# Kernel optimization log

Hardware: AMD Instinct MI355X
Metric: run time of the kernel (lower is better)

The kernel has to match this reference:

```python
import jax, jax.numpy as jnp
import numpy as np

ADAPTIVE_FACTOR = 10  # max(10, num_agents=8)


def _mlp(x, W1, b1, W2, b2, W3, b3):
    h = jax.nn.relu(x @ W1 + b1)
    h = jax.nn.relu(h @ W2 + b2)
    return h @ W3 + b3


def setup_inputs() -> dict:
    key = jax.random.key(0)
    ks = jax.random.split(key, 8)
    B, T, N, D, A = 32, 512, 8, 256, 64
    obs = jax.random.normal(ks[0], (B, T, N, D), dtype=jnp.float32)
    actions = jax.random.uniform(ks[1], (B, T, N, A), dtype=jnp.float32)
    din = D + A
    W1 = jax.random.normal(ks[2], (din, 128), dtype=jnp.float32) / np.sqrt(din)
    b1 = jnp.zeros((128,), dtype=jnp.float32)
    W2 = jax.random.normal(ks[3], (128, 64), dtype=jnp.float32) / np.sqrt(128.0)
    b2 = jnp.zeros((64,), dtype=jnp.float32)
    W3 = jax.random.normal(ks[4], (64, A), dtype=jnp.float32) / np.sqrt(64.0)
    b3 = jnp.zeros((A,), dtype=jnp.float32)
    return {"obs": obs, "actions": actions, "W1": W1, "b1": b1,
            "W2": W2, "b2": b2, "W3": W3, "b3": b3}


def reference(obs, actions, W1, b1, W2, b2, W3, b3):
    # obs: [B,T,N,D], actions: [B,T,N,A]. All agents processed in one batched MLP
    # pass instead of the per-agent Python loop in the original.
    p_with = _mlp(jnp.concatenate([obs, actions], axis=-1), W1, b1, W2, b2, W3, b3)
    p_wo = _mlp(jnp.concatenate([obs, jnp.zeros_like(actions)], axis=-1),
                W1, b1, W2, b2, W3, b3)

    cf_keys = jax.random.split(jax.random.key(42), ADAPTIVE_FACTOR)

    def body(acc, k):
        cf = jax.random.uniform(k, actions.shape, dtype=actions.dtype)
        return acc + _mlp(jnp.concatenate([obs, cf], axis=-1), W1, b1, W2, b2, W3, b3), None

    p_wo, _ = jax.lax.scan(body, p_wo, cf_keys)
    p_wo = p_wo / (ADAPTIVE_FACTOR + 1)

    # F.kl_div(log_softmax(p_with), softmax(p_wo), reduction='none')
    #   = q * (log q - log p)
    logp = jax.nn.log_softmax(p_with, axis=-1)
    logq = jax.nn.log_softmax(p_wo, axis=-1)
    q = jnp.exp(logq)
    influence = q * (logq - logp)          # [B,T,N,A]
    # torch: stack over agents on dim=-1 -> [B,T,A,N], then mean over dim=2 (A)
    return influence.mean(axis=-1)          # [B,T,N]
```

## Files before the change

kernel.cpp:

```cpp
#include <hip/hip_runtime.h>
#include <cstddef>

#define NCF 10

struct TFKeys { unsigned k[2 * NCF]; };

typedef __attribute__((ext_vector_type(8))) _Float16 f16x8;
typedef __attribute__((ext_vector_type(4))) float f32x4;

__host__ __device__ __forceinline__ void tf2x32(unsigned k0, unsigned k1,
                                                unsigned x0, unsigned x1,
                                                unsigned& o0, unsigned& o1) {
  const unsigned ks2 = k0 ^ k1 ^ 0x1BD11BDAu;
  x0 += k0; x1 += k1;
#define TF_R(r) x0 += x1; x1 = (x1 << (r)) | (x1 >> (32 - (r))); x1 ^= x0;
  TF_R(13) TF_R(15) TF_R(26) TF_R(6)
  x0 += k1;  x1 += ks2 + 1u;
  TF_R(17) TF_R(29) TF_R(16) TF_R(24)
  x0 += ks2; x1 += k0 + 2u;
  TF_R(13) TF_R(15) TF_R(26) TF_R(6)
  x0 += k0;  x1 += k1 + 3u;
  TF_R(17) TF_R(29) TF_R(16) TF_R(24)
  x0 += k1;  x1 += ks2 + 4u;
  TF_R(13) TF_R(15) TF_R(26) TF_R(6)
  x0 += ks2; x1 += k0 + 5u;
#undef TF_R
  o0 = x0; o1 = x1;
}

__device__ __forceinline__ float u01(unsigned bits) {
  return __uint_as_float((bits >> 9) | 0x3f800000u) - 1.0f;
}

__device__ __forceinline__ void split44(const float4 a, const float4 b,
                                        f16x8& hh, f16x8& ll) {
  const float v[8] = {a.x, a.y, a.z, a.w, b.x, b.y, b.z, b.w};
#pragma unroll
  for (int e = 0; e < 8; ++e) {
    const _Float16 h = (_Float16)v[e];
    hh[e] = h;
    ll[e] = (_Float16)(v[e] - (float)h);
  }
}

#define MFMA3(acc, ah, al, bh, bl)                                          \
  acc = __builtin_amdgcn_mfma_f32_16x16x32_f16(ah, bh, acc, 0, 0, 0);       \
  acc = __builtin_amdgcn_mfma_f32_16x16x32_f16(ah, bl, acc, 0, 0, 0);       \
  acc = __builtin_amdgcn_mfma_f32_16x16x32_f16(al, bh, acc, 0, 0, 0);

template <int K, int N>
__device__ __forceinline__ void stage_frags(const float* __restrict__ W,
                                            _Float16* fh, _Float16* fl, int t) {
  constexpr int NTN = N / 16;
  for (int i = t; i < K * N; i += 512) {
    const int e = i & 7, lane = (i >> 3) & 63, tile = i >> 9;
    const int kt = tile / NTN, nt = tile % NTN;
    const int k = kt * 32 + ((lane >> 4) << 3) + e;
    const int c = nt * 16 + (lane & 15);
    const float w = W[k * N + c];
    const _Float16 h = (_Float16)w;
    fh[i] = h;
    fl[i] = (_Float16)(w - (float)h);
  }
}

__device__ __forceinline__ int swz(int row, int col) {
  return (row << 5) + (col ^ ((row & 7) << 2));
}

__global__ __launch_bounds__(512, 1)
void infl_fused(const float* __restrict__ obs, const float* __restrict__ actions,
                const float* __restrict__ W1, const float* __restrict__ b1,
                const float* __restrict__ W2, const float* __restrict__ b2,
                const float* __restrict__ W3, const float* __restrict__ b3,
                float* __restrict__ pwbuf, float* __restrict__ out, TFKeys keys) {
  __shared__ __align__(16) unsigned char smem[114688];
  _Float16* w1oh = (_Float16*)smem;
  _Float16* w1ol = (_Float16*)(smem + 32768);
  _Float16* w1h  = (_Float16*)smem;
  _Float16* w1l  = (_Float16*)(smem + 16384);
  _Float16* w2h  = (_Float16*)(smem + 32768);
  _Float16* w2l  = (_Float16*)(smem + 49152);
  _Float16* w3h  = (_Float16*)(smem + 65536);
  _Float16* w3l  = (_Float16*)(smem + 73728);

  const int t = threadIdx.x, wave = t >> 6, lane = t & 63;
  const int R0 = blockIdx.x * 256 + wave * 32;
  const int cA = lane & 15;
  const int kg = (lane >> 4) << 3;
  const int r0 = (lane >> 4) << 2;
  float* cb = (float*)(smem + 81920 + wave * 4096);

  f32x4 ho[2][8];
#pragma unroll
  for (int nt = 0; nt < 8; ++nt) {
    const float bv = b1[nt * 16 + cA];
    ho[0][nt] = (f32x4){bv, bv, bv, bv};
    ho[1][nt] = ho[0][nt];
  }
  {
    const float* orow0 = obs + (size_t)(R0 + cA) * 256;
    const float* orow1 = obs + (size_t)(R0 + 16 + cA) * 256;
    for (int half = 0; half < 2; ++half) {
      __syncthreads();
      stage_frags<128, 128>(W1 + half * 128 * 128, w1oh, w1ol, t);
      __syncthreads();
#pragma unroll
      for (int kt = 0; kt < 4; ++kt) {
        f16x8 oh0, ol0, oh1, ol1;
        {
          const float4 va = *(const float4*)(orow0 + half * 128 + kt * 32 + kg);
          const float4 vb = *(const float4*)(orow0 + half * 128 + kt * 32 + kg + 4);
          split44(va, vb, oh0, ol0);
          const float4 vc = *(const float4*)(orow1 + half * 128 + kt * 32 + kg);
          const float4 vd = *(const float4*)(orow1 + half * 128 + kt * 32 + kg + 4);
          split44(vc, vd, oh1, ol1);
        }
#pragma unroll
        for (int nt = 0; nt < 8; ++nt) {
          const int tile = kt * 8 + nt;
          const f16x8 bh = *(const f16x8*)&w1oh[(tile * 64 + lane) * 8];
          const f16x8 bl = *(const f16x8*)&w1ol[(tile * 64 + lane) * 8];
          MFMA3(ho[0][nt], oh0, ol0, bh, bl)
          MFMA3(ho[1][nt], oh1, ol1, bh, bl)
        }
      }
    }
  }
  __syncthreads();

  stage_frags<64, 128>(W1 + 256 * 128, w1h, w1l, t);
  stage_frags<128, 64>(W2, w2h, w2l, t);
  stage_frags<64, 64>(W3, w3h, w3l, t);

  float b2r[4];
#pragma unroll
  for (int n2 = 0; n2 < 4; ++n2) b2r[n2] = b2[n2 * 16 + cA];
  __syncthreads();

#define MLP_BODY(AH, AL, HAS_ACT, acc3)                                      \
  {                                                                          \
    f32x4 a2[2][4];                                                          \
    _Pragma("unroll") for (int g = 0; g < 2; ++g)                            \
      _Pragma("unroll") for (int n2 = 0; n2 < 4; ++n2)                       \
        a2[g][n2] = (f32x4){b2r[n2], b2r[n2], b2r[n2], b2r[n2]};             \
    _Pragma("unroll") for (int c = 0; c < 4; ++c) {                          \
      f32x4 a10 = ho[0][2 * c], a11 = ho[0][2 * c + 1];                      \
      f32x4 a12 = ho[1][2 * c], a13 = ho[1][2 * c + 1];                      \
      if (HAS_ACT) {                                                         \
        _Pragma("unroll") for (int kt = 0; kt < 2; ++kt) {                   \
          const int t0 = ((kt * 8 + 2 * c) * 64 + lane) * 8;                 \
          const int t1 = ((kt * 8 + 2 * c + 1) * 64 + lane) * 8;             \
          const f16x8 bh0 = *(const f16x8*)&w1h[t0];                         \
          const f16x8 bl0 = *(const f16x8*)&w1l[t0];                         \
          MFMA3(a10, AH[0][kt], AL[0][kt], bh0, bl0)                         \
          MFMA3(a12, AH[1][kt], AL[1][kt], bh0, bl0)                         \
          const f16x8 bh1 = *(const f16x8*)&w1h[t1];                         \
          const f16x8 bl1 = *(const f16x8*)&w1l[t1];                         \
          MFMA3(a11, AH[0][kt], AL[0][kt], bh1, bl1)                         \
          MFMA3(a13, AH[1][kt], AL[1][kt], bh1, bl1)                         \
        }                                                                    \
      }                                                                      \
      _Pragma("unroll") for (int j = 0; j < 4; ++j) {                        \
        cb[swz(r0 + j, cA)]           = fmaxf(a10[j], 0.f);                  \
        cb[swz(r0 + j, 16 + cA)]      = fmaxf(a11[j], 0.f);                  \
        cb[swz(16 + r0 + j, cA)]      = fmaxf(a12[j], 0.f);                  \
        cb[swz(16 + r0 + j, 16 + cA)] = fmaxf(a13[j], 0.f);                  \
      }                                                                      \
      f16x8 hh0, hl0, hh1, hl1;                                              \
      {                                                                      \
        const float4 va = *(const float4*)&cb[swz(cA, kg)];                  \
        const float4 vb = *(const float4*)&cb[swz(cA, kg + 4)];              \
        split44(va, vb, hh0, hl0);                                           \
        const float4 vc = *(const float4*)&cb[swz(16 + cA, kg)];             \
        const float4 vd = *(const float4*)&cb[swz(16 + cA, kg + 4)];         \
        split44(vc, vd, hh1, hl1);                                           \
      }                                                                      \
      _Pragma("unroll") for (int n2 = 0; n2 < 4; ++n2) {                     \
        const int tt = ((c * 4 + n2) * 64 + lane) * 8;                       \
        const f16x8 wh = *(const f16x8*)&w2h[tt];                            \
        const f16x8 wl = *(const f16x8*)&w2l[tt];                            \
        MFMA3(a2[0][n2], hh0, hl0, wh, wl)                                   \
        MFMA3(a2[1][n2], hh1, hl1, wh, wl)                                   \
      }                                                                      \
    }                                                                        \
    _Pragma("unroll") for (int d = 0; d < 2; ++d) {                          \
      _Pragma("unroll") for (int j = 0; j < 4; ++j) {                        \
        cb[swz(r0 + j, cA)]           = fmaxf(a2[0][2 * d][j], 0.f);         \
        cb[swz(r0 + j, 16 + cA)]      = fmaxf(a2[0][2 * d + 1][j], 0.f);     \
        cb[swz(16 + r0 + j, cA)]      = fmaxf(a2[1][2 * d][j], 0.f);         \
        cb[swz(16 + r0 + j, 16 + cA)] = fmaxf(a2[1][2 * d + 1][j], 0.f);     \
      }                                                                      \
      f16x8 hh0, hl0, hh1, hl1;                                              \
      {                                                                      \
        const float4 va = *(const float4*)&cb[swz(cA, kg)];                  \
        const float4 vb = *(const float4*)&cb[swz(cA, kg + 4)];              \
        split44(va, vb, hh0, hl0);                                           \
        const float4 vc = *(const float4*)&cb[swz(16 + cA, kg)];             \
        const float4 vd = *(const float4*)&cb[swz(16 + cA, kg + 4)];         \
        split44(vc, vd, hh1, hl1);                                           \
      }                                                                      \
      _Pragma("unroll") for (int n3 = 0; n3 < 4; ++n3) {                     \
        const int tt = ((d * 4 + n3) * 64 + lane) * 8;                       \
        const f16x8 wh = *(const f16x8*)&w3h[tt];                            \
        const f16x8 wl = *(const f16x8*)&w3l[tt];                            \
        MFMA3(acc3[0][n3], hh0, hl0, wh, wl)                                 \
        MFMA3(acc3[1][n3], hh1, hl1, wh, wl)                                 \
      }                                                                      \
    }                                                                        \
  }

#define GEN_RNG(PP, AH, AL)                                                  \
  {                                                                          \
    const unsigned gk0 = keys.k[2 * ((PP) - 1)];                             \
    const unsigned gk1 = keys.k[2 * ((PP) - 1) + 1];                         \
    _Pragma("unroll") for (int g = 0; g < 2; ++g) {                          \
      const unsigned base = (unsigned)(R0 + g * 16 + cA) * 64u + (unsigned)kg;\
      _Pragma("unroll") for (int kt = 0; kt < 2; ++kt) {                     \
        float v[8];                                                          \
        _Pragma("unroll") for (int e = 0; e < 8; ++e) {                      \
          unsigned o0, o1;                                                   \
          tf2x32(gk0, gk1, 0u, base + (unsigned)(kt * 32 + e), o0, o1);      \
          v[e] = u01(o0 ^ o1);                                               \
        }                                                                    \
        split44(*(const float4*)&v[0], *(const float4*)&v[4],                \
                AH[g][kt], AL[g][kt]);                                       \
      }                                                                      \
    }                                                                        \
  }

  f16x8 aA[2][2], lA[2][2], aB[2][2], lB[2][2];

  {
#pragma unroll
    for (int g = 0; g < 2; ++g) {
      const float* arow = actions + (size_t)(R0 + g * 16 + cA) * 64 + kg;
#pragma unroll
      for (int kt = 0; kt < 2; ++kt) {
        const float4 va = *(const float4*)(arow + kt * 32);
        const float4 vb = *(const float4*)(arow + kt * 32 + 4);
        split44(va, vb, aA[g][kt], lA[g][kt]);
      }
    }
    f32x4 pw[2][4];
#pragma unroll
    for (int g = 0; g < 2; ++g)
#pragma unroll
      for (int nt = 0; nt < 4; ++nt) pw[g][nt] = (f32x4){0.f, 0.f, 0.f, 0.f};
    MLP_BODY(aA, lA, true, pw)
#pragma unroll
    for (int g = 0; g < 2; ++g)
#pragma unroll
      for (int n3 = 0; n3 < 4; ++n3)
#pragma unroll
        for (int j = 0; j < 4; ++j)
          pwbuf[(size_t)(R0 + g * 16 + r0 + j) * 64 + n3 * 16 + cA] =
              pw[g][n3][j];
  }

  f32x4 pacc[2][4];
#pragma unroll
  for (int g = 0; g < 2; ++g)
#pragma unroll
    for (int nt = 0; nt < 4; ++nt) pacc[g][nt] = (f32x4){0.f, 0.f, 0.f, 0.f};

  GEN_RNG(1, aA, lA)
  MLP_BODY(aA, lA, false, pacc)

  for (int i = 0; i < 4; ++i) {
    GEN_RNG(2 * i + 2, aB, lB)
    MLP_BODY(aA, lA, true, pacc)
    GEN_RNG(2 * i + 3, aA, lA)
    MLP_BODY(aB, lB, true, pacc)
  }
  GEN_RNG(10, aB, lB)
  MLP_BODY(aA, lA, true, pacc)
  MLP_BODY(aB, lB, true, pacc)

  const float inv11 = 1.0f / 11.0f;
  float b3r[4];
#pragma unroll
  for (int n3 = 0; n3 < 4; ++n3) b3r[n3] = b3[n3 * 16 + cA];

#pragma unroll
  for (int g = 0; g < 2; ++g) {
#pragma unroll
    for (int j = 0; j < 4; ++j) {
      float pwv[4], pav[4];
#pragma unroll
      for (int nt = 0; nt < 4; ++nt) {
        pwv[nt] = pwbuf[(size_t)(R0 + g * 16 + r0 + j) * 64 + nt * 16 + cA] +
                  b3r[nt];
        pav[nt] = pacc[g][nt][j] * inv11 + b3r[nt];
      }
      float mw = fmaxf(fmaxf(pwv[0], pwv[1]), fmaxf(pwv[2], pwv[3]));
      float ma = fmaxf(fmaxf(pav[0], pav[1]), fmaxf(pav[2], pav[3]));
#pragma unroll
      for (int off = 1; off < 16; off <<= 1) {
        mw = fmaxf(mw, __shfl_xor(mw, off, 64));
        ma = fmaxf(ma, __shfl_xor(ma, off, 64));
      }
      float sw = 0.f, sa = 0.f;
#pragma unroll
      for (int nt = 0; nt < 4; ++nt) {
        sw += expf(pwv[nt] - mw);
        sa += expf(pav[nt] - ma);
      }
#pragma unroll
      for (int off = 1; off < 16; off <<= 1) {
        sw += __shfl_xor(sw, off, 64);
        sa += __shfl_xor(sa, off, 64);
      }
      const float lzw = logf(sw), lza = logf(sa);
      float contrib = 0.f;
#pragma unroll
      for (int nt = 0; nt < 4; ++nt) {
        const float lq = pav[nt] - ma - lza;
        const float lp = pwv[nt] - mw - lzw;
        contrib += expf(lq) * (lq - lp);
      }
#pragma unroll
      for (int off = 1; off < 16; off <<= 1)
        contrib += __shfl_xor(contrib, off, 64);
      if (cA == 0) out[R0 + g * 16 + r0 + j] = contrib * (1.0f / 64.0f);
    }
  }
}

extern "C" void kernel_launch(void* const* d_in, const int* in_sizes, int n_in,
                              void* d_out, int out_size, void* d_ws, size_t ws_size,
                              hipStream_t stream) {
  (void)in_sizes; (void)n_in; (void)ws_size; (void)out_size;
  const float* obs     = (const float*)d_in[0];
  const float* actions = (const float*)d_in[1];
  const float* W1      = (const float*)d_in[2];
  const float* b1      = (const float*)d_in[3];
  const float* W2      = (const float*)d_in[4];
  const float* b2      = (const float*)d_in[5];
  const float* W3      = (const float*)d_in[6];
  const float* b3      = (const float*)d_in[7];

  float* pwbuf = (float*)d_ws;

  TFKeys keys;
  for (unsigned j = 0; j < NCF; ++j) {
    unsigned o0, o1;
    tf2x32(0u, 42u, 0u, j, o0, o1);
    keys.k[2 * j]     = o0;
    keys.k[2 * j + 1] = o1;
  }

  hipLaunchKernelGGL(infl_fused, dim3(512), dim3(512), 0, stream,
                     obs, actions, W1, b1, W2, b2, W3, b3, pwbuf,
                     (float*)d_out, keys);
}
```

Before: 592.1 us.

## Double-buffer per-wave LDS staging and drop RNG/MLP software pipelining

Splits each wave's LDS scratch into two buffers so layer-1 chunk production can run ahead of layer-2 consumption, and the layer-2 to layer-3 handoff writes both halves before reading. The aim is to shorten the LDS write-then-read dependency chains and give the scheduler independent MFMA work between them. Separately, the double-register RNG pipeline (aA/aB) is replaced by a single register set and a non-unrolled loop that generates the next counterfactual after each MLP pass. This lowers register pressure and code size but gives up overlap between RNG generation and MFMA work. LDS per block grows from 112 KB to 144 KB.

```diff
diff --git a/kernel.cpp b/kernel.cpp
--- a/kernel.cpp
+++ b/kernel.cpp
@@ -74,7 +74,7 @@
                 const float* __restrict__ W2, const float* __restrict__ b2,
                 const float* __restrict__ W3, const float* __restrict__ b3,
                 float* __restrict__ pwbuf, float* __restrict__ out, TFKeys keys) {
-  __shared__ __align__(16) unsigned char smem[114688];
+  __shared__ __align__(16) unsigned char smem[147456];
   _Float16* w1oh = (_Float16*)smem;
   _Float16* w1ol = (_Float16*)(smem + 32768);
   _Float16* w1h  = (_Float16*)smem;
@@ -89,7 +89,8 @@
   const int cA = lane & 15;
   const int kg = (lane >> 4) << 3;
   const int r0 = (lane >> 4) << 2;
-  float* cb = (float*)(smem + 81920 + wave * 4096);
+  float* cb0 = (float*)(smem + 81920 + wave * 8192);
+  float* cb1 = cb0 + 1024;
 
   f32x4 ho[2][8];
 #pragma unroll
@@ -138,76 +139,94 @@
   for (int n2 = 0; n2 < 4; ++n2) b2r[n2] = b2[n2 * 16 + cA];
   __syncthreads();
 
+#define L1_PRODUCE(C, BUF, AH, AL, HAS_ACT)                                  \
+  {                                                                          \
+    f32x4 a10 = ho[0][2 * (C)], a11 = ho[0][2 * (C) + 1];                    \
+    f32x4 a12 = ho[1][2 * (C)], a13 = ho[1][2 * (C) + 1];                    \
+    if (HAS_ACT) {                                                           \
+      _Pragma("unroll") for (int kt = 0; kt < 2; ++kt) {                     \
+        const int t0 = ((kt * 8 + 2 * (C)) * 64 + lane) * 8;                 \
+        const int t1 = ((kt * 8 + 2 * (C) + 1) * 64 + lane) * 8;             \
+        const f16x8 bh0 = *(const f16x8*)&w1h[t0];                           \
+        const f16x8 bl0 = *(const f16x8*)&w1l[t0];                           \
+        MFMA3(a10, AH[0][kt], AL[0][kt], bh0, bl0)                           \
+        MFMA3(a12, AH[1][kt], AL[1][kt], bh0, bl0)                           \
+        const f16x8 bh1 = *(const f16x8*)&w1h[t1];                           \
+        const f16x8 bl1 = *(const f16x8*)&w1l[t1];                           \
+        MFMA3(a11, AH[0][kt], AL[0][kt], bh1, bl1)                           \
+        MFMA3(a13, AH[1][kt], AL[1][kt], bh1, bl1)                           \
+      }                                                                      \
+    }                                                                        \
+    _Pragma("unroll") for (int j = 0; j < 4; ++j) {                          \
+      (BUF)[swz(r0 + j, cA)]           = fmaxf(a10[j], 0.f);                 \
+      (BUF)[swz(r0 + j, 16 + cA)]      = fmaxf(a11[j], 0.f);                 \
+      (BUF)[swz(16 + r0 + j, cA)]      = fmaxf(a12[j], 0.f);                 \
+      (BUF)[swz(16 + r0 + j, 16 + cA)] = fmaxf(a13[j], 0.f);                 \
+    }                                                                        \
+  }
+
+#define L2_CONSUME(C, BUF)                                                   \
+  {                                                                          \
+    const float4 va = *(const float4*)&(BUF)[swz(cA, kg)];                   \
+    const float4 vb = *(const float4*)&(BUF)[swz(cA, kg + 4)];               \
+    const float4 vc = *(const float4*)&(BUF)[swz(16 + cA, kg)];              \
+    const float4 vd = *(const float4*)&(BUF)[swz(16 + cA, kg + 4)];          \
+    f16x8 hh0, hl0, hh1, hl1;                                                \
+    split44(va, vb, hh0, hl0);                                               \
+    split44(vc, vd, hh1, hl1);                                               \
+    _Pragma("unroll") for (int n2 = 0; n2 < 4; ++n2) {                       \
+      const int tt = (((C) * 4 + n2) * 64 + lane) * 8;                       \
+      const f16x8 wh = *(const f16x8*)&w2h[tt];                              \
+      const f16x8 wl = *(const f16x8*)&w2l[tt];                              \
+      MFMA3(a2[0][n2], hh0, hl0, wh, wl)                                     \
+      MFMA3(a2[1][n2], hh1, hl1, wh, wl)                                     \
+    }                                                                        \
+  }
+
+#define H2_PRODUCE(D, BUF)                                                   \
+  _Pragma("unroll") for (int j = 0; j < 4; ++j) {                            \
+    (BUF)[swz(r0 + j, cA)]           = fmaxf(a2[0][2 * (D)][j], 0.f);        \
+    (BUF)[swz(r0 + j, 16 + cA)]      = fmaxf(a2[0][2 * (D) + 1][j], 0.f);    \
+    (BUF)[swz(16 + r0 + j, cA)]      = fmaxf(a2[1][2 * (D)][j], 0.f);        \
+    (BUF)[swz(16 + r0 + j, 16 + cA)] = fmaxf(a2[1][2 * (D) + 1][j], 0.f);    \
+  }
+
+#define L3_CONSUME(D, BUF, acc3)                                             \
+  {                                                                          \
+    const float4 va = *(const float4*)&(BUF)[swz(cA, kg)];                   \
+    const float4 vb = *(const float4*)&(BUF)[swz(cA, kg + 4)];               \
+    const float4 vc = *(const float4*)&(BUF)[swz(16 + cA, kg)];              \
+    const float4 vd = *(const float4*)&(BUF)[swz(16 + cA, kg + 4)];          \
+    f16x8 hh0, hl0, hh1, hl1;                                                \
+    split44(va, vb, hh0, hl0);                                               \
+    split44(vc, vd, hh1, hl1);                                               \
+    _Pragma("unroll") for (int n3 = 0; n3 < 4; ++n3) {                       \
+      const int tt = (((D) * 4 + n3) * 64 + lane) * 8;                       \
+      const f16x8 wh = *(const f16x8*)&w3h[tt];                              \
+      const f16x8 wl = *(const f16x8*)&w3l[tt];                              \
+      MFMA3(acc3[0][n3], hh0, hl0, wh, wl)                                   \
+      MFMA3(acc3[1][n3], hh1, hl1, wh, wl)                                   \
+    }                                                                        \
+  }
+
 #define MLP_BODY(AH, AL, HAS_ACT, acc3)                                      \
   {                                                                          \
     f32x4 a2[2][4];                                                          \
     _Pragma("unroll") for (int g = 0; g < 2; ++g)                            \
       _Pragma("unroll") for (int n2 = 0; n2 < 4; ++n2)                       \
         a2[g][n2] = (f32x4){b2r[n2], b2r[n2], b2r[n2], b2r[n2]};             \
-    _Pragma("unroll") for (int c = 0; c < 4; ++c) {                          \
-      f32x4 a10 = ho[0][2 * c], a11 = ho[0][2 * c + 1];                      \
-      f32x4 a12 = ho[1][2 * c], a13 = ho[1][2 * c + 1];                      \
-      if (HAS_ACT) {                                                         \
-        _Pragma("unroll") for (int kt = 0; kt < 2; ++kt) {                   \
-          const int t0 = ((kt * 8 + 2 * c) * 64 + lane) * 8;                 \
-          const int t1 = ((kt * 8 + 2 * c + 1) * 64 + lane) * 8;             \
-          const f16x8 bh0 = *(const f16x8*)&w1h[t0];                         \
-          const f16x8 bl0 = *(const f16x8*)&w1l[t0];                         \
-          MFMA3(a10, AH[0][kt], AL[0][kt], bh0, bl0)                         \
-          MFMA3(a12, AH[1][kt], AL[1][kt], bh0, bl0)                         \
-          const f16x8 bh1 = *(const f16x8*)&w1h[t1];                         \
-          const f16x8 bl1 = *(const f16x8*)&w1l[t1];                         \
-          MFMA3(a11, AH[0][kt], AL[0][kt], bh1, bl1)                         \
-          MFMA3(a13, AH[1][kt], AL[1][kt], bh1, bl1)                         \
-        }                                                                    \
-      }                                                                      \
-      _Pragma("unroll") for (int j = 0; j < 4; ++j) {                        \
-        cb[swz(r0 + j, cA)]           = fmaxf(a10[j], 0.f);                  \
-        cb[swz(r0 + j, 16 + cA)]      = fmaxf(a11[j], 0.f);                  \
-        cb[swz(16 + r0 + j, cA)]      = fmaxf(a12[j], 0.f);                  \
-        cb[swz(16 + r0 + j, 16 + cA)] = fmaxf(a13[j], 0.f);                  \
-      }                                                                      \
-      f16x8 hh0, hl0, hh1, hl1;                                              \
-      {                                                                      \
-        const float4 va = *(const float4*)&cb[swz(cA, kg)];                  \
-        const float4 vb = *(const float4*)&cb[swz(cA, kg + 4)];              \
-        split44(va, vb, hh0, hl0);                                           \
-        const float4 vc = *(const float4*)&cb[swz(16 + cA, kg)];             \
-        const float4 vd = *(const float4*)&cb[swz(16 + cA, kg + 4)];         \
-        split44(vc, vd, hh1, hl1);                                           \
-      }                                                                      \
-      _Pragma("unroll") for (int n2 = 0; n2 < 4; ++n2) {                     \
-        const int tt = ((c * 4 + n2) * 64 + lane) * 8;                       \
-        const f16x8 wh = *(const f16x8*)&w2h[tt];                            \
-        const f16x8 wl = *(const f16x8*)&w2l[tt];                            \
-        MFMA3(a2[0][n2], hh0, hl0, wh, wl)                                   \
-        MFMA3(a2[1][n2], hh1, hl1, wh, wl)                                   \
-      }                                                                      \
-    }                                                                        \
-    _Pragma("unroll") for (int d = 0; d < 2; ++d) {                          \
-      _Pragma("unroll") for (int j = 0; j < 4; ++j) {                        \
-        cb[swz(r0 + j, cA)]           = fmaxf(a2[0][2 * d][j], 0.f);         \
-        cb[swz(r0 + j, 16 + cA)]      = fmaxf(a2[0][2 * d + 1][j], 0.f);     \
-        cb[swz(16 + r0 + j, cA)]      = fmaxf(a2[1][2 * d][j], 0.f);         \
-        cb[swz(16 + r0 + j, 16 + cA)] = fmaxf(a2[1][2 * d + 1][j], 0.f);     \
-      }                                                                      \
-      f16x8 hh0, hl0, hh1, hl1;                                              \
-      {                                                                      \
-        const float4 va = *(const float4*)&cb[swz(cA, kg)];                  \
-        const float4 vb = *(const float4*)&cb[swz(cA, kg + 4)];              \
-        split44(va, vb, hh0, hl0);                                           \
-        const float4 vc = *(const float4*)&cb[swz(16 + cA, kg)];             \
-        const float4 vd = *(const float4*)&cb[swz(16 + cA, kg + 4)];         \
-        split44(vc, vd, hh1, hl1);                                           \
-      }                                                                      \
-      _Pragma("unroll") for (int n3 = 0; n3 < 4; ++n3) {                     \
-        const int tt = ((d * 4 + n3) * 64 + lane) * 8;                       \
-        const f16x8 wh = *(const f16x8*)&w3h[tt];                            \
-        const f16x8 wl = *(const f16x8*)&w3l[tt];                            \
-        MFMA3(acc3[0][n3], hh0, hl0, wh, wl)                                 \
-        MFMA3(acc3[1][n3], hh1, hl1, wh, wl)                                 \
-      }                                                                      \
-    }                                                                        \
+    L1_PRODUCE(0, cb0, AH, AL, HAS_ACT)                                      \
+    L1_PRODUCE(1, cb1, AH, AL, HAS_ACT)                                      \
+    L2_CONSUME(0, cb0)                                                       \
+    L1_PRODUCE(2, cb0, AH, AL, HAS_ACT)                                      \
+    L2_CONSUME(1, cb1)                                                       \
+    L1_PRODUCE(3, cb1, AH, AL, HAS_ACT)                                      \
+    L2_CONSUME(2, cb0)                                                       \
+    L2_CONSUME(3, cb1)                                                       \
+    H2_PRODUCE(0, cb0)                                                       \
+    H2_PRODUCE(1, cb1)                                                       \
+    L3_CONSUME(0, cb0, acc3)                                                 \
+    L3_CONSUME(1, cb1, acc3)                                                 \
   }
 
 #define GEN_RNG(PP, AH, AL)                                                  \
@@ -229,7 +248,7 @@
     }                                                                        \
   }
 
-  f16x8 aA[2][2], lA[2][2], aB[2][2], lB[2][2];
+  f16x8 ah[2][2], al[2][2];
 
   {
 #pragma unroll
@@ -239,7 +258,7 @@
       for (int kt = 0; kt < 2; ++kt) {
         const float4 va = *(const float4*)(arow + kt * 32);
         const float4 vb = *(const float4*)(arow + kt * 32 + 4);
-        split44(va, vb, aA[g][kt], lA[g][kt]);
+        split44(va, vb, ah[g][kt], al[g][kt]);
       }
     }
     f32x4 pw[2][4];
@@ -247,7 +266,7 @@
     for (int g = 0; g < 2; ++g)
 #pragma unroll
       for (int nt = 0; nt < 4; ++nt) pw[g][nt] = (f32x4){0.f, 0.f, 0.f, 0.f};
-    MLP_BODY(aA, lA, true, pw)
+    MLP_BODY(ah, al, true, pw)
 #pragma unroll
     for (int g = 0; g < 2; ++g)
 #pragma unroll
@@ -264,18 +283,13 @@
 #pragma unroll
     for (int nt = 0; nt < 4; ++nt) pacc[g][nt] = (f32x4){0.f, 0.f, 0.f, 0.f};
 
-  GEN_RNG(1, aA, lA)
-  MLP_BODY(aA, lA, false, pacc)
-
-  for (int i = 0; i < 4; ++i) {
-    GEN_RNG(2 * i + 2, aB, lB)
-    MLP_BODY(aA, lA, true, pacc)
-    GEN_RNG(2 * i + 3, aA, lA)
-    MLP_BODY(aB, lB, true, pacc)
-  }
-  GEN_RNG(10, aB, lB)
-  MLP_BODY(aA, lA, true, pacc)
-  MLP_BODY(aB, lB, true, pacc)
+  GEN_RNG(1, ah, al)
+  MLP_BODY(ah, al, false, pacc)
+#pragma unroll 1
+  for (int p = 1; p <= 10; ++p) {
+    MLP_BODY(ah, al, true, pacc)
+    if (p < 10) GEN_RNG(p + 1, ah, al)
+  }
 
   const float inv11 = 1.0f / 11.0f;
   float b3r[4];
```

After: 579.2 us. -2.2%, faster.
